# Optimization experiments

Measured on AMD Instinct MI355X. Metric: run time of the kernel, lower is better.

## Reference

```python
import jax, jax.numpy as jnp
import numpy as np

T, D, H, E, K = 2048, 1024, 512, 16, 4  # tokens, d_model, d_expert, n_experts, top_k


def setup_inputs() -> dict:
    key = jax.random.key(0)
    ks = jax.random.split(key, 5)
    x = jax.random.normal(ks[0], (T, D), dtype=jnp.float32)
    centroids = jax.random.normal(ks[1], (E, D), dtype=jnp.float32) * 0.006
    bias = jnp.zeros((E,), dtype=jnp.float32)  # router bias buffer (aux_loss=True adds it)
    w_gate = jax.random.normal(ks[2], (E, D, H), dtype=jnp.float32) * (1.0 / np.sqrt(D))
    w_up = jax.random.normal(ks[3], (E, D, H), dtype=jnp.float32) * (1.0 / np.sqrt(D))
    w_down = jax.random.normal(ks[4], (E, H, D), dtype=jnp.float32) * (1.0 / np.sqrt(H))
    scale = jnp.ones((1,), dtype=jnp.float32) * 0.1
    return {"x": x, "centroids": centroids, "bias": bias,
            "w_gate": w_gate, "w_up": w_up, "w_down": w_down, "scale": scale}


def reference(x, centroids, bias, w_gate, w_up, w_down, scale):
    n_exp = w_gate.shape[0]
    # Router: sigmoid(x @ C^T + bias), top-k, gates normalized to sum 1.
    logits = x @ centroids.T + bias                      # [T, E]
    scores = jax.nn.sigmoid(logits)
    gates, idx = jax.lax.top_k(scores, K)                # [T, K]
    gates = gates / jnp.clip(gates.sum(axis=-1, keepdims=True), 1e-9)
    # Scatter gates into dense per-expert combine weights [T, E]
    # (top-k indices are unique per token, so one_hot-sum == scatter-set).
    combine = jnp.sum(jax.nn.one_hot(idx, n_exp, dtype=x.dtype) * gates[..., None], axis=1)
    # SwiGLU per expert, weighted by combine gates (zero gate => zero contribution,
    # identical math to the per-expert gather/index_add_ loop).
    h = jax.nn.silu(jnp.einsum('td,edh->teh', x, w_gate)) * jnp.einsum('td,edh->teh', x, w_up)
    h = h * combine[:, :, None]                          # [T, E, H]
    out = jnp.einsum('teh,ehd->td', h, w_down) * scale   # [T, D]
    return out
```

## Files before the change

### kernel.cpp

```cpp
#include <hip/hip_runtime.h>
#include <hip/hip_bf16.h>

#define T_TOK 2048
#define DMODEL 1024
#define HEXP 512
#define NEXP 16
#define TOPK 4
#define CAP 2048

typedef __attribute__((ext_vector_type(4))) float f32x4;
typedef __attribute__((ext_vector_type(8))) short short8;
typedef __attribute__((ext_vector_type(4))) unsigned short ush4;
typedef __attribute__((ext_vector_type(8))) unsigned short ush8;
typedef __attribute__((ext_vector_type(4))) int i32x4;
typedef __attribute__((ext_vector_type(4))) unsigned int u32x4;

static __device__ __forceinline__ unsigned short f2bf(float f) {
  union { float f; unsigned int u; } v; v.f = f;
  unsigned int r = v.u + 0x7FFFu + ((v.u >> 16) & 1u);
  return (unsigned short)(r >> 16);
}

static __device__ __forceinline__ void gl16(const unsigned short* g, unsigned short* l) {
  __builtin_amdgcn_global_load_lds(
      (const __attribute__((address_space(1))) unsigned int*)g,
      (__attribute__((address_space(3))) unsigned int*)l, 16, 0, 0);
}

#define SWZ128(r, kb) (((r) << 7) + ((((kb) >> 3) ^ ((r) & 15)) << 3))

__global__ __launch_bounds__(256) void prep(const float* __restrict__ w_gate,
                                            const float* __restrict__ w_up,
                                            const float* __restrict__ w_down,
                                            unsigned short* __restrict__ wgT,
                                            unsigned short* __restrict__ wuT,
                                            unsigned short* __restrict__ wdT,
                                            const float* __restrict__ x,
                                            const float* __restrict__ cen,
                                            const float* __restrict__ bias,
                                            unsigned short* __restrict__ xbf,
                                            int* __restrict__ selIdx,
                                            float* __restrict__ selGate) {
  int blk = (int)blockIdx.x;
  if (blk >= 512) {
    __shared__ unsigned int ldsT[64][33];
    int idx = blk - 512;
    int sel = idx >> 11, bb = idx & 2047;
    const float* in; unsigned short* out; int R, C, rx, cy, e;
    if (sel == 0)      { in = w_gate; out = wgT; R = 1024; C = 512;
                         rx = bb & 15; cy = (bb >> 4) & 7; e = bb >> 7; }
    else if (sel == 1) { in = w_up;   out = wuT; R = 1024; C = 512;
                         rx = bb & 15; cy = (bb >> 4) & 7; e = bb >> 7; }
    else               { in = w_down; out = wdT; R = 512;  C = 1024;
                         rx = bb & 7;  cy = (bb >> 3) & 15; e = bb >> 7; }
    in  += (size_t)e * R * C;
    out += (size_t)e * R * C;
    int r0 = rx * 64, c0 = cy * 64;
    int tid = (int)threadIdx.x;
    int cc = (tid & 15) * 4;
    int pp = tid >> 4;
#pragma unroll
    for (int i = 0; i < 2; i++) {
      int p = pp + i * 16;
      int r = 2 * p;
      f32x4 va = *(const f32x4*)(in + (size_t)(r0 + r) * C + c0 + cc);
      f32x4 vb = *(const f32x4*)(in + (size_t)(r0 + r + 1) * C + c0 + cc);
#pragma unroll
      for (int k = 0; k < 4; k++) {
        unsigned int pk = (unsigned int)f2bf(va[k]) | ((unsigned int)f2bf(vb[k]) << 16);
        ldsT[cc + k][p] = pk;
      }
    }
    __syncthreads();
    int oc = tid >> 2;
    int sblk = (tid & 3) * 8;
    unsigned int q[8];
#pragma unroll
    for (int k = 0; k < 8; k++) q[k] = ldsT[oc][sblk + k];
    unsigned short* op = out + (size_t)(c0 + oc) * R + r0 + sblk * 2;
    *(u32x4*)(op)     = *(u32x4*)&q[0];
    *(u32x4*)(op + 8) = *(u32x4*)&q[4];
  } else {
    int tid = (int)threadIdx.x;
    int lane = tid & 63, wid = tid >> 6;
    int t = blk * 4 + wid;
    const float* xr = x + (size_t)t * DMODEL;
    f32x4 xv[4];
#pragma unroll
    for (int i = 0; i < 4; i++) xv[i] = *(const f32x4*)(xr + i * 256 + lane * 4);
    unsigned short* xb = xbf + (size_t)t * DMODEL;
#pragma unroll
    for (int i = 0; i < 4; i++) {
      ush4 b = { f2bf(xv[i][0]), f2bf(xv[i][1]), f2bf(xv[i][2]), f2bf(xv[i][3]) };
      *(ush4*)(xb + i * 256 + lane * 4) = b;
    }
    float p[16];
#pragma unroll
    for (int e = 0; e < NEXP; e++) p[e] = 0.f;
#pragma unroll
    for (int e = 0; e < NEXP; e++) {
      const float* ce = cen + (size_t)e * DMODEL;
#pragma unroll
      for (int i = 0; i < 4; i++) {
        f32x4 cv = *(const f32x4*)(ce + i * 256 + lane * 4);
#pragma unroll
        for (int j = 0; j < 4; j++) p[e] = fmaf(xv[i][j], cv[j], p[e]);
      }
    }
#pragma unroll
    for (int o = 32; o >= 1; o >>= 1) {
#pragma unroll
      for (int e = 0; e < NEXP; e++) p[e] += __shfl_xor(p[e], o);
    }
    float s[16];
#pragma unroll
    for (int e = 0; e < NEXP; e++) s[e] = 1.f / (1.f + expf(-(p[e] + bias[e])));
    int sel[4]; float val[4]; float gsum = 0.f;
#pragma unroll
    for (int k = 0; k < 4; k++) {
      float best = -1e30f; int bi = 0;
#pragma unroll
      for (int e = 0; e < NEXP; e++) {
        if (s[e] > best) { best = s[e]; bi = e; }
      }
      sel[k] = bi; val[k] = best; gsum += best;
#pragma unroll
      for (int e = 0; e < NEXP; e++) if (e == bi) s[e] = -1e30f;
    }
    float inv = 1.f / fmaxf(gsum, 1e-9f);
    if (lane == 0) {
      i32x4 si = { sel[0], sel[1], sel[2], sel[3] };
      f32x4 sg = { val[0] * inv, val[1] * inv, val[2] * inv, val[3] * inv };
      *(i32x4*)&selIdx[t * 4] = si;
      *(f32x4*)&selGate[t * 4] = sg;
    }
  }
}

__global__ __launch_bounds__(256) void buildlists(const int* __restrict__ selIdx,
                                                  const float* __restrict__ selGate,
                                                  int* __restrict__ cnt,
                                                  int* __restrict__ listTok,
                                                  float* __restrict__ listGate,
                                                  int* __restrict__ listSlot) {
  int e = blockIdx.x;
  int tid = (int)threadIdx.x, lane = tid & 63, w = tid >> 6;
  int i0 = tid * 32;
  int vals[32];
#pragma unroll
  for (int j = 0; j < 8; j++)
    *(i32x4*)&vals[j * 4] = *(const i32x4*)&selIdx[i0 + j * 4];
  int mycount = 0;
#pragma unroll
  for (int j = 0; j < 32; j++) mycount += (vals[j] == e) ? 1 : 0;
  int s = mycount;
#pragma unroll
  for (int o = 1; o < 64; o <<= 1) {
    int n = __shfl_up(s, o);
    if (lane >= o) s += n;
  }
  __shared__ int wtot[4];
  if (lane == 63) wtot[w] = s;
  __syncthreads();
  int wbase = 0;
#pragma unroll
  for (int j = 0; j < 4; j++) wbase += (j < w) ? wtot[j] : 0;
  int pos = wbase + s - mycount;
#pragma unroll
  for (int j = 0; j < 32; j++) {
    if (vals[j] == e) {
      int i = i0 + j;
      listTok[e * CAP + pos]  = i >> 2;
      listGate[e * CAP + pos] = selGate[i];
      listSlot[e * CAP + pos] = i;
      pos++;
    }
  }
  if (tid == 255) cnt[e] = pos;
}

__global__ __launch_bounds__(512) void ffn1(const unsigned short* __restrict__ xbf,
                                            const unsigned short* __restrict__ wgT,
                                            const unsigned short* __restrict__ wuT,
                                            const int* __restrict__ cnt,
                                            const int* __restrict__ listTok,
                                            const float* __restrict__ listGate,
                                            unsigned short* __restrict__ hbuf) {
  int b = (int)blockIdx.x;
  int xcd = b & 7, slot = b >> 3;
  int e = xcd + 8 * (slot >> 7);
  int tile = slot & 127;
  int my = tile >> 3;
  int nx = tile & 7;
  int c = cnt[e];
  int m0 = my * 128;
  if (m0 >= c) return;
  int n0 = nx * 64;
  __shared__ unsigned short sA[16384];
  __shared__ unsigned short sG[8192];
  __shared__ unsigned short sU[8192];
  __shared__ int sTok[128];
  __shared__ float sGate[128];
  int tid = (int)threadIdx.x;
  if (tid < 128) {
    int r = m0 + tid;
    sTok[tid]  = (r < c) ? listTok[e * CAP + r] : listTok[e * CAP];
    sGate[tid] = (r < c) ? listGate[e * CAP + r] : 0.f;
  }
  __syncthreads();
  int lane = tid & 63, wid = tid >> 6;
  int wr = wid >> 1, wc = wid & 1;
  const unsigned short* wg = wgT + ((size_t)e * HEXP + n0) * DMODEL;
  const unsigned short* wu = wuT + ((size_t)e * HEXP + n0) * DMODEL;
  int rl = lane >> 4;
  int lg = lane & 15;
  const unsigned short* pA[4];
#pragma unroll
  for (int i = 0; i < 4; i++) {
    int lr = wid * 16 + i * 4 + rl;
    int cg = lg ^ (lr & 15);
    pA[i] = xbf + (size_t)sTok[lr] * DMODEL + cg * 8;
  }
  const unsigned short* pG[2];
  const unsigned short* pU[2];
#pragma unroll
  for (int j = 0; j < 2; j++) {
    int lr = wid * 8 + j * 4 + rl;
    int cg = lg ^ (lr & 15);
    pG[j] = wg + (size_t)lr * DMODEL + cg * 8;
    pU[j] = wu + (size_t)lr * DMODEL + cg * 8;
  }
  f32x4 ag[2][2] = {{{0,0,0,0},{0,0,0,0}},{{0,0,0,0},{0,0,0,0}}};
  f32x4 au[2][2] = {{{0,0,0,0},{0,0,0,0}},{{0,0,0,0},{0,0,0,0}}};
#pragma unroll 1
  for (int k0 = 0; k0 < DMODEL; k0 += 128) {
    __syncthreads();
#pragma unroll
    for (int i = 0; i < 4; i++)
      gl16(pA[i] + k0, sA + (wid * 16 + i * 4) * 128);
#pragma unroll
    for (int j = 0; j < 2; j++) {
      gl16(pG[j] + k0, sG + (wid * 8 + j * 4) * 128);
      gl16(pU[j] + k0, sU + (wid * 8 + j * 4) * 128);
    }
    __syncthreads();
#pragma unroll
    for (int kk = 0; kk < 4; kk++) {
      int kb = (kk << 5) + (rl << 3);
      short8 a[2], g[2], u[2];
#pragma unroll
      for (int m = 0; m < 2; m++)
        a[m] = *(const short8*)&sA[SWZ128((wr << 5) + lg + m * 16, kb)];
#pragma unroll
      for (int n = 0; n < 2; n++) {
        g[n] = *(const short8*)&sG[SWZ128((wc << 5) + lg + n * 16, kb)];
        u[n] = *(const short8*)&sU[SWZ128((wc << 5) + lg + n * 16, kb)];
      }
#pragma unroll
      for (int m = 0; m < 2; m++) {
#pragma unroll
        for (int n = 0; n < 2; n++) {
          ag[m][n] = __builtin_amdgcn_mfma_f32_16x16x32_bf16(a[m], g[n], ag[m][n], 0, 0, 0);
          au[m][n] = __builtin_amdgcn_mfma_f32_16x16x32_bf16(a[m], u[n], au[m][n], 0, 0, 0);
        }
      }
    }
  }
  int rlo = (lane >> 4) << 2;
  int cl = lane & 15;
#pragma unroll
  for (int m = 0; m < 2; m++) {
#pragma unroll
    for (int r = 0; r < 4; r++) {
      int row = (wr << 5) + m * 16 + rlo + r;
      int grow = m0 + row;
      if (grow < c) {
        float gwt = sGate[row];
#pragma unroll
        for (int n = 0; n < 2; n++) {
          int col = n0 + (wc << 5) + n * 16 + cl;
          float g = ag[m][n][r];
          float u = au[m][n][r];
          float sig = 1.f / (1.f + __expf(-g));
          float h = g * sig * u * gwt;
          hbuf[((size_t)e * CAP + grow) * HEXP + col] = f2bf(h);
        }
      }
    }
  }
}

__global__ __launch_bounds__(512) void ffn2(const unsigned short* __restrict__ hbuf,
                                            const unsigned short* __restrict__ wdT,
                                            const int* __restrict__ cnt,
                                            const int* __restrict__ listSlot,
                                            float* __restrict__ y) {
  int b = (int)blockIdx.x;
  int xcd = b & 7, slot = b >> 3;
  int e = xcd + 8 * (slot >> 7);
  int tile = slot & 127;
  int my = tile >> 3;
  int nx = tile & 7;
  int c = cnt[e];
  int m0 = my * 128;
  if (m0 >= c) return;
  int n0 = nx * 128;
  __shared__ unsigned short sA[16384];
  __shared__ unsigned short sB[16384];
  __shared__ int sSlot[128];
  int tid = (int)threadIdx.x;
  if (tid < 128) {
    int r = m0 + tid;
    sSlot[tid] = (r < c) ? listSlot[e * CAP + r] : 0;
  }
  __syncthreads();
  int lane = tid & 63, wid = tid >> 6;
  int wr = wid >> 1, wc = wid & 1;
  const unsigned short* ha = hbuf + ((size_t)e * CAP + m0) * HEXP;
  const unsigned short* wd = wdT + ((size_t)e * DMODEL + n0) * HEXP;
  int rl = lane >> 4;
  int lg = lane & 15;
  const unsigned short* pA[4];
  const unsigned short* pB[4];
#pragma unroll
  for (int i = 0; i < 4; i++) {
    int lr = wid * 16 + i * 4 + rl;
    int cg = lg ^ (lr & 15);
    pA[i] = ha + (size_t)lr * HEXP + cg * 8;
    pB[i] = wd + (size_t)lr * HEXP + cg * 8;
  }
  f32x4 acc[2][4];
#pragma unroll
  for (int m = 0; m < 2; m++)
#pragma unroll
    for (int n = 0; n < 4; n++) acc[m][n] = f32x4{0, 0, 0, 0};
#pragma unroll 1
  for (int k0 = 0; k0 < HEXP; k0 += 128) {
    __syncthreads();
#pragma unroll
    for (int i = 0; i < 4; i++) {
      gl16(pA[i] + k0, sA + (wid * 16 + i * 4) * 128);
      gl16(pB[i] + k0, sB + (wid * 16 + i * 4) * 128);
    }
    __syncthreads();
#pragma unroll
    for (int kk = 0; kk < 4; kk++) {
      int kb = (kk << 5) + (rl << 3);
      short8 a[2], bb[4];
#pragma unroll
      for (int m = 0; m < 2; m++)
        a[m] = *(const short8*)&sA[SWZ128((wr << 5) + lg + m * 16, kb)];
#pragma unroll
      for (int n = 0; n < 4; n++)
        bb[n] = *(const short8*)&sB[SWZ128((wc << 6) + lg + n * 16, kb)];
#pragma unroll
      for (int m = 0; m < 2; m++) {
#pragma unroll
        for (int n = 0; n < 4; n++)
          acc[m][n] = __builtin_amdgcn_mfma_f32_16x16x32_bf16(a[m], bb[n], acc[m][n], 0, 0, 0);
      }
    }
  }
  int rlo = (lane >> 4) << 2;
  int cl = lane & 15;
#pragma unroll
  for (int m = 0; m < 2; m++) {
#pragma unroll
    for (int r = 0; r < 4; r++) {
      int row = (wr << 5) + m * 16 + rlo + r;
      int grow = m0 + row;
      if (grow < c) {
        int slot2 = sSlot[row];
#pragma unroll
        for (int n = 0; n < 4; n++) {
          int col = n0 + (wc << 6) + n * 16 + cl;
          y[(size_t)slot2 * DMODEL + col] = acc[m][n][r];
        }
      }
    }
  }
}

__global__ __launch_bounds__(256) void reducek(const float* __restrict__ y,
                                               const float* __restrict__ scale,
                                               float* __restrict__ out) {
  int i = blockIdx.x * 256 + (int)threadIdx.x;
  int t = i >> 8;
  int d = (i & 255) << 2;
  const float* yb = y + (size_t)t * 4 * DMODEL + d;
  f32x4 s = *(const f32x4*)(yb);
  s += *(const f32x4*)(yb + DMODEL);
  s += *(const f32x4*)(yb + 2 * DMODEL);
  s += *(const f32x4*)(yb + 3 * DMODEL);
  float sc = scale[0];
  s *= sc;
  *(f32x4*)(out + (size_t)t * DMODEL + d) = s;
}

extern "C" void kernel_launch(void* const* d_in, const int* in_sizes, int n_in,
                              void* d_out, int out_size, void* d_ws, size_t ws_size,
                              hipStream_t stream) {
  const float* x      = (const float*)d_in[0];
  const float* cen    = (const float*)d_in[1];
  const float* bias   = (const float*)d_in[2];
  const float* w_gate = (const float*)d_in[3];
  const float* w_up   = (const float*)d_in[4];
  const float* w_down = (const float*)d_in[5];
  const float* scale  = (const float*)d_in[6];
  float* out = (float*)d_out;

  char* ws = (char*)d_ws;
  unsigned short* xbf  = (unsigned short*)(ws);
  unsigned short* wgT  = (unsigned short*)(ws + 4194304);
  unsigned short* wuT  = (unsigned short*)(ws + 20971520);
  unsigned short* wdT  = (unsigned short*)(ws + 37748736);
  unsigned short* hbuf = (unsigned short*)(ws + 54525952);
  float*          y    = (float*)(ws + 88080384);
  int*            cnt  = (int*)(ws + 121634816);
  int*        listTok  = (int*)(ws + 121635072);
  float*     listGate  = (float*)(ws + 121766144);
  int*       listSlot  = (int*)(ws + 121897216);
  int*         selIdx  = (int*)(ws + 122028288);
  float*      selGate  = (float*)(ws + 122061056);

  prep<<<dim3(6656), 256, 0, stream>>>(w_gate, w_up, w_down, wgT, wuT, wdT,
                                       x, cen, bias, xbf, selIdx, selGate);
  buildlists<<<dim3(16), 256, 0, stream>>>(selIdx, selGate, cnt, listTok, listGate, listSlot);
  ffn1<<<dim3(2048), 512, 0, stream>>>(xbf, wgT, wuT, cnt, listTok, listGate, hbuf);
  ffn2<<<dim3(2048), 512, 0, stream>>>(hbuf, wdT, cnt, listSlot, y);
  reducek<<<dim3(2048), 256, 0, stream>>>(y, scale, out);
}
```

Baseline: 98.60 us.

## Double-buffer LDS tiles with async prefetch in both expert GEMM kernels

Both the SwiGLU up-projection and the down-projection GEMM now stage K in 64-wide slices across two LDS buffers. The next slice is issued via global_load_lds while the current one is consumed, and explicit vmcnt waits and barriers replace the previous load-then-sync-then-compute loop. The aim is to hide global memory latency behind MFMA work. In exchange there are more barriers per K step and the buffer slices are smaller, and correctness depends on the hand-written vmcnt counts matching the outstanding loads.

```diff
diff --git a/kernel.cpp b/kernel.cpp
--- a/kernel.cpp
+++ b/kernel.cpp
@@ -27,7 +27,11 @@
       (__attribute__((address_space(3))) unsigned int*)l, 16, 0, 0);
 }
 
-#define SWZ128(r, kb) (((r) << 7) + ((((kb) >> 3) ^ ((r) & 15)) << 3))
+#define SWZ(r, kb) (((r) << 6) + ((((kb) >> 3) ^ ((r) & 7)) << 3))
+
+#define WAITV4 asm volatile("s_waitcnt vmcnt(4)" ::: "memory")
+#define WAITV0 asm volatile("s_waitcnt vmcnt(0)" ::: "memory")
+#define BAR __builtin_amdgcn_s_barrier()
 
 __global__ __launch_bounds__(256) void prep(const float* __restrict__ w_gate,
                                             const float* __restrict__ w_up,
@@ -196,9 +200,9 @@
   int m0 = my * 128;
   if (m0 >= c) return;
   int n0 = nx * 64;
-  __shared__ unsigned short sA[16384];
-  __shared__ unsigned short sG[8192];
-  __shared__ unsigned short sU[8192];
+  __shared__ unsigned short sA[2][8192];
+  __shared__ unsigned short sG[2][4096];
+  __shared__ unsigned short sU[2][4096];
   __shared__ int sTok[128];
   __shared__ float sGate[128];
   int tid = (int)threadIdx.x;
@@ -212,60 +216,71 @@
   int wr = wid >> 1, wc = wid & 1;
   const unsigned short* wg = wgT + ((size_t)e * HEXP + n0) * DMODEL;
   const unsigned short* wu = wuT + ((size_t)e * HEXP + n0) * DMODEL;
-  int rl = lane >> 4;
-  int lg = lane & 15;
-  const unsigned short* pA[4];
-#pragma unroll
-  for (int i = 0; i < 4; i++) {
-    int lr = wid * 16 + i * 4 + rl;
-    int cg = lg ^ (lr & 15);
-    pA[i] = xbf + (size_t)sTok[lr] * DMODEL + cg * 8;
-  }
-  const unsigned short* pG[2];
-  const unsigned short* pU[2];
-#pragma unroll
-  for (int j = 0; j < 2; j++) {
-    int lr = wid * 8 + j * 4 + rl;
-    int cg = lg ^ (lr & 15);
-    pG[j] = wg + (size_t)lr * DMODEL + cg * 8;
-    pU[j] = wu + (size_t)lr * DMODEL + cg * 8;
-  }
+  int rloc = lane >> 3;
+  int lg8 = lane & 7;
+  const unsigned short* pA[2];
+#pragma unroll
+  for (int i = 0; i < 2; i++) {
+    int row = wid * 16 + i * 8 + rloc;
+    int cg = lg8 ^ (row & 7);
+    pA[i] = xbf + (size_t)sTok[row] * DMODEL + cg * 8;
+  }
+  int rG = wid * 8 + rloc;
+  const unsigned short* pG = wg + (size_t)rG * DMODEL + (lg8 ^ (rG & 7)) * 8;
+  const unsigned short* pU = wu + (size_t)rG * DMODEL + (lg8 ^ (rG & 7)) * 8;
+  int rl = lane >> 4, lg = lane & 15;
   f32x4 ag[2][2] = {{{0,0,0,0},{0,0,0,0}},{{0,0,0,0},{0,0,0,0}}};
   f32x4 au[2][2] = {{{0,0,0,0},{0,0,0,0}},{{0,0,0,0},{0,0,0,0}}};
+
+#define FFN1_STAGE(B, K0)                                         \
+  do {                                                            \
+    gl16(pA[0] + (K0), &sA[B][(wid * 16) * 64]);                  \
+    gl16(pA[1] + (K0), &sA[B][(wid * 16 + 8) * 64]);              \
+    gl16(pG + (K0), &sG[B][(wid * 8) * 64]);                      \
+    gl16(pU + (K0), &sU[B][(wid * 8) * 64]);                      \
+  } while (0)
+
+#define FFN1_COMP(B)                                                              \
+  do {                                                                            \
+    _Pragma("unroll")                                                             \
+    for (int kk = 0; kk < 2; kk++) {                                              \
+      int kb = (kk << 5) + (rl << 3);                                             \
+      short8 a[2], g[2], u[2];                                                    \
+      _Pragma("unroll")                                                           \
+      for (int m = 0; m < 2; m++)                                                 \
+        a[m] = *(const short8*)&sA[B][SWZ((wr << 5) + lg + m * 16, kb)];          \
+      _Pragma("unroll")                                                           \
+      for (int n = 0; n < 2; n++) {                                               \
+        g[n] = *(const short8*)&sG[B][SWZ((wc << 5) + lg + n * 16, kb)];          \
+        u[n] = *(const short8*)&sU[B][SWZ((wc << 5) + lg + n * 16, kb)];          \
+      }                                                                           \
+      _Pragma("unroll")                                                           \
+      for (int m = 0; m < 2; m++) {                                               \
+        _Pragma("unroll")                                                         \
+        for (int n = 0; n < 2; n++) {                                             \
+          ag[m][n] = __builtin_amdgcn_mfma_f32_16x16x32_bf16(a[m], g[n], ag[m][n], 0, 0, 0); \
+          au[m][n] = __builtin_amdgcn_mfma_f32_16x16x32_bf16(a[m], u[n], au[m][n], 0, 0, 0); \
+        }                                                                         \
+      }                                                                           \
+    }                                                                             \
+  } while (0)
+
+  FFN1_STAGE(0, 0);
+  FFN1_STAGE(1, 64);
 #pragma unroll 1
-  for (int k0 = 0; k0 < DMODEL; k0 += 128) {
-    __syncthreads();
-#pragma unroll
-    for (int i = 0; i < 4; i++)
-      gl16(pA[i] + k0, sA + (wid * 16 + i * 4) * 128);
-#pragma unroll
-    for (int j = 0; j < 2; j++) {
-      gl16(pG[j] + k0, sG + (wid * 8 + j * 4) * 128);
-      gl16(pU[j] + k0, sU + (wid * 8 + j * 4) * 128);
-    }
-    __syncthreads();
-#pragma unroll
-    for (int kk = 0; kk < 4; kk++) {
-      int kb = (kk << 5) + (rl << 3);
-      short8 a[2], g[2], u[2];
-#pragma unroll
-      for (int m = 0; m < 2; m++)
-        a[m] = *(const short8*)&sA[SWZ128((wr << 5) + lg + m * 16, kb)];
-#pragma unroll
-      for (int n = 0; n < 2; n++) {
-        g[n] = *(const short8*)&sG[SWZ128((wc << 5) + lg + n * 16, kb)];
-        u[n] = *(const short8*)&sU[SWZ128((wc << 5) + lg + n * 16, kb)];
-      }
-#pragma unroll
-      for (int m = 0; m < 2; m++) {
-#pragma unroll
-        for (int n = 0; n < 2; n++) {
-          ag[m][n] = __builtin_amdgcn_mfma_f32_16x16x32_bf16(a[m], g[n], ag[m][n], 0, 0, 0);
-          au[m][n] = __builtin_amdgcn_mfma_f32_16x16x32_bf16(a[m], u[n], au[m][n], 0, 0, 0);
-        }
-      }
-    }
-  }
+  for (int t = 0; t < 16; t += 2) {
+    if (t < 15) WAITV4; else WAITV0;
+    BAR;
+    FFN1_COMP(0);
+    BAR;
+    if (t + 2 < 16) FFN1_STAGE(0, (t + 2) * 64);
+    if (t + 1 < 15) WAITV4; else WAITV0;
+    BAR;
+    FFN1_COMP(1);
+    BAR;
+    if (t + 3 < 16) FFN1_STAGE(1, (t + 3) * 64);
+  }
+
   int rlo = (lane >> 4) << 2;
   int cl = lane & 15;
 #pragma unroll
@@ -305,8 +320,8 @@
   int m0 = my * 128;
   if (m0 >= c) return;
   int n0 = nx * 128;
-  __shared__ unsigned short sA[16384];
-  __shared__ unsigned short sB[16384];
+  __shared__ unsigned short sA[2][8192];
+  __shared__ unsigned short sB[2][8192];
   __shared__ int sSlot[128];
   int tid = (int)threadIdx.x;
   if (tid < 128) {
@@ -318,49 +333,68 @@
   int wr = wid >> 1, wc = wid & 1;
   const unsigned short* ha = hbuf + ((size_t)e * CAP + m0) * HEXP;
   const unsigned short* wd = wdT + ((size_t)e * DMODEL + n0) * HEXP;
-  int rl = lane >> 4;
-  int lg = lane & 15;
-  const unsigned short* pA[4];
-  const unsigned short* pB[4];
-#pragma unroll
-  for (int i = 0; i < 4; i++) {
-    int lr = wid * 16 + i * 4 + rl;
-    int cg = lg ^ (lr & 15);
-    pA[i] = ha + (size_t)lr * HEXP + cg * 8;
-    pB[i] = wd + (size_t)lr * HEXP + cg * 8;
-  }
+  int rloc = lane >> 3, lg8 = lane & 7;
+  const unsigned short* pA[2];
+  const unsigned short* pB[2];
+#pragma unroll
+  for (int i = 0; i < 2; i++) {
+    int row = wid * 16 + i * 8 + rloc;
+    int cg = lg8 ^ (row & 7);
+    pA[i] = ha + (size_t)row * HEXP + cg * 8;
+    pB[i] = wd + (size_t)row * HEXP + cg * 8;
+  }
+  int rl = lane >> 4, lg = lane & 15;
   f32x4 acc[2][4];
 #pragma unroll
   for (int m = 0; m < 2; m++)
 #pragma unroll
     for (int n = 0; n < 4; n++) acc[m][n] = f32x4{0, 0, 0, 0};
+
+#define FFN2_STAGE(B, K0)                                   \
+  do {                                                      \
+    gl16(pA[0] + (K0), &sA[B][(wid * 16) * 64]);            \
+    gl16(pA[1] + (K0), &sA[B][(wid * 16 + 8) * 64]);        \
+    gl16(pB[0] + (K0), &sB[B][(wid * 16) * 64]);            \
+    gl16(pB[1] + (K0), &sB[B][(wid * 16 + 8) * 64]);        \
+  } while (0)
+
+#define FFN2_COMP(B)                                                              \
+  do {                                                                            \
+    _Pragma("unroll")                                                             \
+    for (int kk = 0; kk < 2; kk++) {                                              \
+      int kb = (kk << 5) + (rl << 3);                                             \
+      short8 a[2], bb[4];                                                         \
+      _Pragma("unroll")                                                           \
+      for (int m = 0; m < 2; m++)                                                 \
+        a[m] = *(const short8*)&sA[B][SWZ((wr << 5) + lg + m * 16, kb)];          \
+      _Pragma("unroll")                                                           \
+      for (int n = 0; n < 4; n++)                                                 \
+        bb[n] = *(const short8*)&sB[B][SWZ((wc << 6) + lg + n * 16, kb)];         \
+      _Pragma("unroll")                                                           \
+      for (int m = 0; m < 2; m++) {                                               \
+        _Pragma("unroll")                                                         \
+        for (int n = 0; n < 4; n++)                                               \
+          acc[m][n] = __builtin_amdgcn_mfma_f32_16x16x32_bf16(a[m], bb[n], acc[m][n], 0, 0, 0); \
+      }                                                                           \
+    }                                                                             \
+  } while (0)
+
+  FFN2_STAGE(0, 0);
+  FFN2_STAGE(1, 64);
 #pragma unroll 1
-  for (int k0 = 0; k0 < HEXP; k0 += 128) {
-    __syncthreads();
-#pragma unroll
-    for (int i = 0; i < 4; i++) {
-      gl16(pA[i] + k0, sA + (wid * 16 + i * 4) * 128);
-      gl16(pB[i] + k0, sB + (wid * 16 + i * 4) * 128);
-    }
-    __syncthreads();
-#pragma unroll
-    for (int kk = 0; kk < 4; kk++) {
-      int kb = (kk << 5) + (rl << 3);
-      short8 a[2], bb[4];
-#pragma unroll
-      for (int m = 0; m < 2; m++)
-        a[m] = *(const short8*)&sA[SWZ128((wr << 5) + lg + m * 16, kb)];
-#pragma unroll
-      for (int n = 0; n < 4; n++)
-        bb[n] = *(const short8*)&sB[SWZ128((wc << 6) + lg + n * 16, kb)];
-#pragma unroll
-      for (int m = 0; m < 2; m++) {
-#pragma unroll
-        for (int n = 0; n < 4; n++)
-          acc[m][n] = __builtin_amdgcn_mfma_f32_16x16x32_bf16(a[m], bb[n], acc[m][n], 0, 0, 0);
-      }
-    }
-  }
+  for (int t = 0; t < 8; t += 2) {
+    if (t < 7) WAITV4; else WAITV0;
+    BAR;
+    FFN2_COMP(0);
+    BAR;
+    if (t + 2 < 8) FFN2_STAGE(0, (t + 2) * 64);
+    if (t + 1 < 7) WAITV4; else WAITV0;
+    BAR;
+    FFN2_COMP(1);
+    BAR;
+    if (t + 3 < 8) FFN2_STAGE(1, (t + 3) * 64);
+  }
+
   int rlo = (lane >> 4) << 2;
   int cl = lane & 15;
 #pragma unroll
```

Result: slower. 100.6 us (+2.1%).
